# Kernel optimization log

Hardware: AMD Instinct MI355X
Metric: run time of the kernel (lower is better)

## Reference

```python
import jax, jax.numpy as jnp
import numpy as np

N_KNOTS = 16384
BATCH = 256
N_SAMP = 32768


def setup_inputs() -> dict:
    key = jax.random.key(0)
    k1, k2, k3 = jax.random.split(key, 3)
    # strictly increasing knot abscissae (matches module assumption of sorted x_points)
    incs = jax.random.uniform(k1, (N_KNOTS,), minval=0.01, maxval=1.0, dtype=jnp.float32)
    x_points = jnp.cumsum(incs)
    y_points = jax.random.normal(k2, (N_KNOTS,), dtype=jnp.float32)
    # samples must have a valid right bracket: x in [x_points[0], x_points[N-2])
    lo = x_points[0]
    hi = x_points[N_KNOTS - 2]
    u = jax.random.uniform(k3, (BATCH, N_SAMP), dtype=jnp.float32)
    x_samp = lo + u * (hi - lo) * 0.999
    return {"x_samp": x_samp, "x_points": x_points, "y_points": y_points}


def reference(x_samp, x_points, y_points):
    # Original: masked argmin over (x_samp - x_points) with negatives set to inf,
    # i.e. index of the largest knot <= x_samp. Equivalent to searchsorted(right)-1.
    idxi = jnp.searchsorted(x_points, x_samp, side='right') - 1  # [B, S]
    idxf = idxi + 1
    xi = x_points[idxi]  # [B, S] gather
    xf = x_points[idxf]
    yi = y_points[idxi]
    yf = y_points[idxf]
    ds = (x_samp - xi) / (xf - xi)
    return yi + ds * (yf - yi)
```

## Files before the change

kernel.cpp:

```cpp
#include <hip/hip_runtime.h>


#define NB 14336
#define NKMAX 16384
#define PAD 16

typedef float    f32x4 __attribute__((ext_vector_type(4)));
typedef unsigned u32x4 __attribute__((ext_vector_type(4)));

__device__ __forceinline__ int bucket_of(float v, float lo, float inv_w) {
    return (int)((v - lo) * inv_w);
}

__device__ __forceinline__ unsigned pack_ys(float y, float s) {
    _Float16 hy = (_Float16)y, hs = (_Float16)s;
    unsigned short uy = __builtin_bit_cast(unsigned short, hy);
    unsigned short us = __builtin_bit_cast(unsigned short, hs);
    return (unsigned)uy | ((unsigned)us << 16);
}

__device__ __forceinline__ float lerp_ys(float dx, unsigned u) {
    float hy = (float)__builtin_bit_cast(_Float16, (unsigned short)(u & 0xffffu));
    float hs = (float)__builtin_bit_cast(_Float16, (unsigned short)(u >> 16));
    return fmaf(dx, hs, hy);
}

__global__ void build_tbl(const float* __restrict__ xp, const float* __restrict__ yp,
                          unsigned* __restrict__ ysg, unsigned short* __restrict__ tbl,
                          int nk) {
    int i = blockIdx.x * blockDim.x + threadIdx.x;
    float lo = xp[0];
    float inv_w = (float)NB / (xp[nk - 1] - lo);
    if (i < nk) {
        float y0 = yp[i];
        float slope = 0.0f;
        if (i < nk - 1) slope = (yp[i + 1] - y0) / (xp[i + 1] - xp[i]);
        ysg[i] = pack_ys(y0, slope);
    }
    if (i < NB) {
        int v = 0;
        if (i > 0) {
            int loj = -1, hij = nk - 1;
            while (loj < hij) {
                int mid = (loj + hij + 1) >> 1;
                if (bucket_of(xp[mid], lo, inv_w) <= i - 1) loj = mid; else hij = mid - 1;
            }
            v = loj < 0 ? 0 : (loj > nk - 2 ? nk - 2 : loj);
        }
        tbl[i] = (unsigned short)v;
    }
}

__global__ __launch_bounds__(1024) void interp(
        const f32x4* __restrict__ xs4, const float* __restrict__ xp,
        const unsigned* __restrict__ ysg, const unsigned short* __restrict__ tbl,
        f32x4* __restrict__ out4, int n4, int nk) {
    __shared__ __align__(16) float sx[NKMAX + PAD];
    __shared__ __align__(16) unsigned sys[NKMAX + PAD];
    __shared__ unsigned short sT[NB];

    {
        const f32x4* xp4 = (const f32x4*)xp;
        f32x4* sx4w = (f32x4*)sx;
        for (int i = threadIdx.x; i < nk / 4; i += 1024) sx4w[i] = xp4[i];
        const u32x4* ysg4 = (const u32x4*)ysg;
        u32x4* sys4w = (u32x4*)sys;
        for (int i = threadIdx.x; i < nk / 4; i += 1024) sys4w[i] = ysg4[i];
        for (int i = threadIdx.x; i < NB; i += 1024) sT[i] = tbl[i];
        if (threadIdx.x < PAD) {
            sx[nk + threadIdx.x] = __builtin_inff();
            sys[nk + threadIdx.x] = 0u;
        }
    }

    float lo = xp[0];
    float inv_w = (float)NB / (xp[nk - 1] - lo);
    __syncthreads();

    const f32x4* sx4 = (const f32x4*)sx;
    const u32x4* sys4 = (const u32x4*)sys;

    int tid = blockIdx.x * blockDim.x + threadIdx.x;
    int T = gridDim.x * blockDim.x;

    int t = tid;
    f32x4 xa, xb;
    bool has1 = (t < n4), has2 = (t + T < n4);
    if (has1) xa = __builtin_nontemporal_load(&xs4[t]);
    if (has2) xb = __builtin_nontemporal_load(&xs4[t + T]);

    while (has1) {
        int tn = t + 2 * T;
        f32x4 xan, xbn;
        bool h1n = (tn < n4), h2n = (tn + T < n4);
        if (h1n) xan = __builtin_nontemporal_load(&xs4[tn]);
        if (h2n) xbn = __builtin_nontemporal_load(&xs4[tn + T]);

        f32x4 res[2];
        #pragma unroll
        for (int half = 0; half < 2; half++) {
            f32x4 xq = (half == 0) ? xa : xb;
            float x[4] = {xq.x, xq.y, xq.z, xq.w};
            int al[4];
            f32x4 wx0[4], wx1[4];
            u32x4 wy0[4], wy1[4];
            #pragma unroll
            for (int k = 0; k < 4; k++) {
                int b = bucket_of(x[k], lo, inv_w);
                b = min(max(b, 0), NB - 1);
                al[k] = ((int)sT[b]) & ~3;
                int q = al[k] >> 2;
                wx0[k] = sx4[q];
                wx1[k] = sx4[q + 1];
                wy0[k] = sys4[q];
                wy1[k] = sys4[q + 1];
            }
            #pragma unroll
            for (int k = 0; k < 4; k++) {
                float xk = x[k];
                float xi = wx0[k].x; unsigned ys = wy0[k].x;
                if (wx0[k].y <= xk) { xi = wx0[k].y; ys = wy0[k].y; }
                if (wx0[k].z <= xk) { xi = wx0[k].z; ys = wy0[k].z; }
                if (wx0[k].w <= xk) { xi = wx0[k].w; ys = wy0[k].w; }
                if (wx1[k].x <= xk) { xi = wx1[k].x; ys = wy1[k].x; }
                if (wx1[k].y <= xk) { xi = wx1[k].y; ys = wy1[k].y; }
                if (wx1[k].z <= xk) { xi = wx1[k].z; ys = wy1[k].z; }
                bool tail = (wx1[k].w <= xk);
                if (tail) { xi = wx1[k].w; ys = wy1[k].w; }
                if (tail) {
                    int j = al[k] + 7;
                    while (sx[j + 1] <= xk) j++;
                    xi = sx[j]; ys = sys[j];
                }
                res[half][k] = lerp_ys(xk - xi, ys);
            }
        }
        __builtin_nontemporal_store(res[0], &out4[t]);
        if (has2) __builtin_nontemporal_store(res[1], &out4[t + T]);

        t = tn; xa = xan; xb = xbn; has1 = h1n; has2 = h2n;
    }
}

extern "C" void kernel_launch(void* const* d_in, const int* in_sizes, int n_in,
                              void* d_out, int out_size, void* d_ws, size_t ws_size,
                              hipStream_t stream) {
    const float* xs = (const float*)d_in[0];
    const float* xp = (const float*)d_in[1];
    const float* yp = (const float*)d_in[2];
    int ns = in_sizes[0];
    int nk = in_sizes[1];

    unsigned* ysg = (unsigned*)d_ws;
    unsigned short* tbl = (unsigned short*)((char*)d_ws + (size_t)nk * sizeof(unsigned));

    int na = (nk > NB ? nk : NB);
    build_tbl<<<(na + 255) / 256, 256, 0, stream>>>(xp, yp, ysg, tbl, nk);

    int n4 = ns / 4;
    interp<<<256, 1024, 0, stream>>>((const f32x4*)xs, xp, ysg, tbl,
                                     (f32x4*)d_out, n4, nk);
}
```

Baseline: 106.9 us.

## Interleave knot x and packed y/slope into records, shrink bracket window

Stores each knot as an (x, packed half y/slope) pair in one interleaved shared-memory array instead of two separate arrays. The bucket count is raised so each bucket spans fewer knots, and the lookup now reads four unaligned 8-byte records from the table start instead of two aligned 16-byte vectors from each array. This cuts LDS reads and compare/select work per sample, but more samples may fall into the serial tail-scan loop when a bucket holds more knots than the window. The bucket table also grows, so more LDS is used per block.

```diff
diff --git a/kernel.cpp b/kernel.cpp
--- a/kernel.cpp
+++ b/kernel.cpp
@@ -1,41 +1,49 @@
 #include <hip/hip_runtime.h>
 
 
-#define NB 14336
+#define NB 16256
 #define NKMAX 16384
-#define PAD 16
+#define PADR 4
+#define NREC (NKMAX + PADR)
 
-typedef float    f32x4 __attribute__((ext_vector_type(4)));
-typedef unsigned u32x4 __attribute__((ext_vector_type(4)));
+typedef float f32x4 __attribute__((ext_vector_type(4)));
+typedef float f32x2 __attribute__((ext_vector_type(2)));
 
 __device__ __forceinline__ int bucket_of(float v, float lo, float inv_w) {
     return (int)((v - lo) * inv_w);
 }
 
-__device__ __forceinline__ unsigned pack_ys(float y, float s) {
+__device__ __forceinline__ float pack_ys_f(float y, float s) {
     _Float16 hy = (_Float16)y, hs = (_Float16)s;
     unsigned short uy = __builtin_bit_cast(unsigned short, hy);
     unsigned short us = __builtin_bit_cast(unsigned short, hs);
-    return (unsigned)uy | ((unsigned)us << 16);
+    unsigned u = (unsigned)uy | ((unsigned)us << 16);
+    return __builtin_bit_cast(float, u);
 }
 
-__device__ __forceinline__ float lerp_ys(float dx, unsigned u) {
+__device__ __forceinline__ float lerp_ys(float dx, float ysf) {
+    unsigned u = __builtin_bit_cast(unsigned, ysf);
     float hy = (float)__builtin_bit_cast(_Float16, (unsigned short)(u & 0xffffu));
     float hs = (float)__builtin_bit_cast(_Float16, (unsigned short)(u >> 16));
     return fmaf(dx, hs, hy);
 }
 
 __global__ void build_tbl(const float* __restrict__ xp, const float* __restrict__ yp,
-                          unsigned* __restrict__ ysg, unsigned short* __restrict__ tbl,
+                          float* __restrict__ recg, unsigned short* __restrict__ tbl,
                           int nk) {
     int i = blockIdx.x * blockDim.x + threadIdx.x;
     float lo = xp[0];
     float inv_w = (float)NB / (xp[nk - 1] - lo);
-    if (i < nk) {
-        float y0 = yp[i];
-        float slope = 0.0f;
-        if (i < nk - 1) slope = (yp[i + 1] - y0) / (xp[i + 1] - xp[i]);
-        ysg[i] = pack_ys(y0, slope);
+    if (i < nk + PADR) {
+        float x, y, s;
+        if (i < nk) {
+            x = xp[i]; y = yp[i];
+            s = (i < nk - 1) ? (yp[i + 1] - y) / (xp[i + 1] - x) : 0.0f;
+        } else {
+            x = __builtin_inff(); y = 0.0f; s = 0.0f;
+        }
+        recg[2 * i]     = x;
+        recg[2 * i + 1] = pack_ys_f(y, s);
     }
     if (i < NB) {
         int v = 0;
@@ -53,32 +61,24 @@
 
 __global__ __launch_bounds__(1024) void interp(
         const f32x4* __restrict__ xs4, const float* __restrict__ xp,
-        const unsigned* __restrict__ ysg, const unsigned short* __restrict__ tbl,
+        const float* __restrict__ recg, const unsigned short* __restrict__ tbl,
         f32x4* __restrict__ out4, int n4, int nk) {
-    __shared__ __align__(16) float sx[NKMAX + PAD];
-    __shared__ __align__(16) unsigned sys[NKMAX + PAD];
+    __shared__ __align__(16) float srec[NREC * 2];
     __shared__ unsigned short sT[NB];
 
     {
-        const f32x4* xp4 = (const f32x4*)xp;
-        f32x4* sx4w = (f32x4*)sx;
-        for (int i = threadIdx.x; i < nk / 4; i += 1024) sx4w[i] = xp4[i];
-        const u32x4* ysg4 = (const u32x4*)ysg;
-        u32x4* sys4w = (u32x4*)sys;
-        for (int i = threadIdx.x; i < nk / 4; i += 1024) sys4w[i] = ysg4[i];
+        const f32x4* rg4 = (const f32x4*)recg;
+        f32x4* sr4 = (f32x4*)srec;
+        int n = (NREC * 2) / 4;
+        for (int i = threadIdx.x; i < n; i += 1024) sr4[i] = rg4[i];
         for (int i = threadIdx.x; i < NB; i += 1024) sT[i] = tbl[i];
-        if (threadIdx.x < PAD) {
-            sx[nk + threadIdx.x] = __builtin_inff();
-            sys[nk + threadIdx.x] = 0u;
-        }
     }
 
     float lo = xp[0];
     float inv_w = (float)NB / (xp[nk - 1] - lo);
     __syncthreads();
 
-    const f32x4* sx4 = (const f32x4*)sx;
-    const u32x4* sys4 = (const u32x4*)sys;
+    const f32x2* sr2 = (const f32x2*)srec;
 
     int tid = blockIdx.x * blockDim.x + threadIdx.x;
     int T = gridDim.x * blockDim.x;
@@ -101,36 +101,29 @@
         for (int half = 0; half < 2; half++) {
             f32x4 xq = (half == 0) ? xa : xb;
             float x[4] = {xq.x, xq.y, xq.z, xq.w};
-            int al[4];
-            f32x4 wx0[4], wx1[4];
-            u32x4 wy0[4], wy1[4];
+            int base[4];
+            f32x2 r0[4], r1[4], r2[4], r3[4];
             #pragma unroll
             for (int k = 0; k < 4; k++) {
                 int b = bucket_of(x[k], lo, inv_w);
-                b = min(max(b, 0), NB - 1);
-                al[k] = ((int)sT[b]) & ~3;
-                int q = al[k] >> 2;
-                wx0[k] = sx4[q];
-                wx1[k] = sx4[q + 1];
-                wy0[k] = sys4[q];
-                wy1[k] = sys4[q + 1];
+                b = min(b, NB - 1);
+                base[k] = (int)sT[b];
+                r0[k] = sr2[base[k]];
+                r1[k] = sr2[base[k] + 1];
+                r2[k] = sr2[base[k] + 2];
+                r3[k] = sr2[base[k] + 3];
             }
             #pragma unroll
             for (int k = 0; k < 4; k++) {
                 float xk = x[k];
-                float xi = wx0[k].x; unsigned ys = wy0[k].x;
-                if (wx0[k].y <= xk) { xi = wx0[k].y; ys = wy0[k].y; }
-                if (wx0[k].z <= xk) { xi = wx0[k].z; ys = wy0[k].z; }
-                if (wx0[k].w <= xk) { xi = wx0[k].w; ys = wy0[k].w; }
-                if (wx1[k].x <= xk) { xi = wx1[k].x; ys = wy1[k].x; }
-                if (wx1[k].y <= xk) { xi = wx1[k].y; ys = wy1[k].y; }
-                if (wx1[k].z <= xk) { xi = wx1[k].z; ys = wy1[k].z; }
-                bool tail = (wx1[k].w <= xk);
-                if (tail) { xi = wx1[k].w; ys = wy1[k].w; }
+                float xi = r0[k].x, ys = r0[k].y;
+                if (r1[k].x <= xk) { xi = r1[k].x; ys = r1[k].y; }
+                if (r2[k].x <= xk) { xi = r2[k].x; ys = r2[k].y; }
+                bool tail = (r3[k].x <= xk);
                 if (tail) {
-                    int j = al[k] + 7;
-                    while (sx[j + 1] <= xk) j++;
-                    xi = sx[j]; ys = sys[j];
+                    int j = base[k] + 3;
+                    while (srec[2 * (j + 1)] <= xk) j++;
+                    xi = srec[2 * j]; ys = srec[2 * j + 1];
                 }
                 res[half][k] = lerp_ys(xk - xi, ys);
             }
@@ -151,13 +144,13 @@
     int ns = in_sizes[0];
     int nk = in_sizes[1];
 
-    unsigned* ysg = (unsigned*)d_ws;
-    unsigned short* tbl = (unsigned short*)((char*)d_ws + (size_t)nk * sizeof(unsigned));
+    float* recg = (float*)d_ws;
+    unsigned short* tbl = (unsigned short*)((char*)d_ws + (size_t)NREC * 2 * sizeof(float));
 
-    int na = (nk > NB ? nk : NB);
-    build_tbl<<<(na + 255) / 256, 256, 0, stream>>>(xp, yp, ysg, tbl, nk);
+    int na = (nk + PADR > NB ? nk + PADR : NB);
+    build_tbl<<<(na + 255) / 256, 256, 0, stream>>>(xp, yp, recg, tbl, nk);
 
     int n4 = ns / 4;
-    interp<<<256, 1024, 0, stream>>>((const f32x4*)xs, xp, ysg, tbl,
+    interp<<<256, 1024, 0, stream>>>((const f32x4*)xs, xp, recg, tbl,
                                      (f32x4*)d_out, n4, nk);
 }
```

After: 105.5 us. Within noise of the previous version (-1.3%).
